# Optimization experiments

Measured on AMD Instinct MI355X. Metric: run time of the kernel, lower is better.

The kernel has to match this reference:

```python
import jax, jax.numpy as jnp
import numpy as np
import math

D_MODEL = 1024
D_STATE = 16
D_CONV = 4
EXPAND = 2
D_INNER = EXPAND * D_MODEL  # 2048
DT_RANK = 64
B_SZ = 2
L_SEQ = 1024


def setup_inputs() -> dict:
    key = jax.random.key(0)
    ks = jax.random.split(key, 10)
    x = jax.random.normal(ks[0], (B_SZ, L_SEQ, D_MODEL), dtype=jnp.float32)
    in_proj_w = jax.random.normal(ks[1], (2 * D_INNER, D_MODEL), dtype=jnp.float32) * (1.0 / math.sqrt(D_MODEL))
    conv_w = jax.random.normal(ks[2], (D_INNER, 1, D_CONV), dtype=jnp.float32) * (1.0 / math.sqrt(D_CONV))
    conv_b = jax.random.normal(ks[3], (D_INNER,), dtype=jnp.float32) * 0.01
    x_proj_w = jax.random.normal(ks[4], (DT_RANK + 2 * D_STATE, D_INNER), dtype=jnp.float32) * (1.0 / math.sqrt(D_INNER))
    dt_init_std = DT_RANK ** (-0.5)
    dt_proj_w = jax.random.uniform(ks[5], (D_INNER, DT_RANK), dtype=jnp.float32, minval=-dt_init_std, maxval=dt_init_std)
    dt = jnp.exp(jax.random.uniform(ks[6], (D_INNER,), dtype=jnp.float32) * (math.log(0.1) - math.log(0.001)) + math.log(0.001))
    dt = jnp.clip(dt, 1e-4, None)
    dt_proj_b = dt + jnp.log(-jnp.expm1(-dt))
    A_log = jnp.log(jnp.tile(jnp.arange(1, D_STATE + 1, dtype=jnp.float32)[None, :], (D_INNER, 1)))
    D = jnp.ones((D_INNER,), dtype=jnp.float32)
    out_proj_w = jax.random.normal(ks[7], (D_MODEL, D_INNER), dtype=jnp.float32) * (1.0 / math.sqrt(D_INNER))
    return {"x": x, "in_proj_w": in_proj_w, "conv_w": conv_w, "conv_b": conv_b,
            "x_proj_w": x_proj_w, "dt_proj_w": dt_proj_w, "dt_proj_b": dt_proj_b,
            "A_log": A_log, "D": D, "out_proj_w": out_proj_w}


def _mamba_forward(x, in_proj_w, conv_w, conv_b, x_proj_w, dt_proj_w, dt_proj_b, A_log, D, out_proj_w):
    B, L, _ = x.shape
    # input projection -> x, z each [B, L, Di]
    xz = jnp.einsum('bld,ed->ble', x, in_proj_w)
    xs, z = jnp.split(xz, 2, axis=-1)
    # causal depthwise conv along L (torch pads K-1 both sides then trims -> left pad only)
    xc = jnp.transpose(xs, (0, 2, 1))  # [B, Di, L]
    xc = jax.lax.conv_general_dilated(
        xc, conv_w, window_strides=(1,), padding=[(D_CONV - 1, 0)],
        feature_group_count=D_INNER, dimension_numbers=('NCH', 'OIH', 'NCH'))
    xc = xc + conv_b[None, :, None]
    xs = jnp.transpose(xc, (0, 2, 1))  # [B, L, Di]
    xs = jax.nn.silu(xs)
    # SSM parameters
    A = -jnp.exp(A_log)  # [Di, N]
    dbc = jnp.einsum('bld,ed->ble', xs, x_proj_w)
    delta_r = dbc[..., :DT_RANK]
    Bm = dbc[..., DT_RANK:DT_RANK + D_STATE]       # [B, L, N]
    Cm = dbc[..., DT_RANK + D_STATE:]              # [B, L, N]
    delta = jnp.einsum('blr,dr->bld', delta_r, dt_proj_w)
    delta = jax.nn.softplus(delta + dt_proj_b)     # [B, L, Di]
    # selective scan: h_t = exp(delta*A)*h_{t-1} + delta*B*x
    dA = jnp.exp(delta[..., None] * A)                          # [B, L, Di, N]
    dBx = (delta * xs)[..., None] * Bm[:, :, None, :]           # [B, L, Di, N]
    dA_t = jnp.moveaxis(dA, 1, 0)    # [L, B, Di, N]
    dBx_t = jnp.moveaxis(dBx, 1, 0)
    C_t = jnp.moveaxis(Cm, 1, 0)     # [L, B, N]
    h0 = jnp.zeros((B, D_INNER, D_STATE), dtype=xs.dtype)

    def step(h, inp):
        da, bx, c = inp
        h = da * h + bx
        y = jnp.einsum('bdn,bn->bd', h, c)
        return h, y

    _, ys = jax.lax.scan(step, h0, (dA_t, dBx_t, C_t))
    y = jnp.moveaxis(ys, 0, 1)       # [B, L, Di]
    y = y + D * xs
    # gating and output projection
    out = y * jax.nn.silu(z)
    return jnp.einsum('bld,od->blo', out, out_proj_w)


def reference(x, in_proj_w, conv_w, conv_b, x_proj_w, dt_proj_w, dt_proj_b, A_log, D, out_proj_w):
    return _mamba_forward(x, in_proj_w, conv_w, conv_b, x_proj_w, dt_proj_w, dt_proj_b, A_log, D, out_proj_w)
```

## Files before the change

### kernel.cpp

```cpp
#include <hip/hip_runtime.h>
#include <hip/hip_bf16.h>

typedef __attribute__((ext_vector_type(8))) short short8;
typedef __attribute__((ext_vector_type(4))) float f32x4;
typedef __hip_bfloat16 bf16;

#define D_MODEL 1024
#define D_INNER 2048
#define DT_RANK 64
#define D_STATE 16
#define B_SZ 2
#define L_SEQ 1024
#define NSEG 64
#define SL 16

__device__ __forceinline__ float b2f(bf16 x){ return __bfloat162float(x); }
__device__ __forceinline__ bf16  f2b(float x){ return __float2bfloat16(x); }

__device__ __forceinline__ void cvt_store8(bf16* dst, const float* s){
  union { short8 v; bf16 e[8]; } u;
  #pragma unroll
  for (int i = 0; i < 8; i++) u.e[i] = f2b(s[i]);
  *(short8*)dst = u.v;
}

__device__ __forceinline__ void gl_lds16(const bf16* g, bf16* l){
  __builtin_amdgcn_global_load_lds((const __attribute__((address_space(1))) unsigned int*)g,
                                   (__attribute__((address_space(3))) unsigned int*)l, 16, 0, 0);
}

__global__ __launch_bounds__(256) void cvt5_k(const float* s0, bf16* d0, int c0,
                                              const float* s1, bf16* d1, int c1,
                                              const float* s2, bf16* d2, int c2,
                                              const float* s3, bf16* d3, int c3,
                                              const float* s4, bf16* d4, int c4)
{
  int i = blockIdx.x * 256 + threadIdx.x;
  const float* s; bf16* d; int off;
  if      (i < c0) { s = s0; d = d0; off = i; }
  else if (i < c1) { s = s1; d = d1; off = i - c0; }
  else if (i < c2) { s = s2; d = d2; off = i - c1; }
  else if (i < c3) { s = s3; d = d3; off = i - c2; }
  else if (i < c4) { s = s4; d = d4; off = i - c3; }
  else return;
  float b[8];
  *(float4*)&b[0] = *(const float4*)(s + (size_t)off * 8);
  *(float4*)&b[4] = *(const float4*)(s + (size_t)off * 8 + 4);
  cvt_store8(d + (size_t)off * 8, b);
}

template<int MODE, int JT>
__global__ __launch_bounds__(256) void gemm_glds(const bf16* __restrict__ A,
                                                 const bf16* __restrict__ B,
                                                 void* __restrict__ Cout,
                                                 const float* __restrict__ bias,
                                                 int M, int N, int K)
{
  constexpr int BN = JT * 32;
  constexpr int BI = BN / 64;
  __shared__ bf16 As[128 * 32];
  __shared__ bf16 Bs[BN * 32];
  const int bm = blockIdx.y * 128, bn = blockIdx.x * BN;
  const int tid  = threadIdx.x;
  const int lane = tid & 63, wave = tid >> 6;
  const int wm = (wave & 1) * 64, wn = (wave >> 1) * (JT * 16);
  const int r = lane & 15, q = lane >> 4;

  const bf16* asrc[2];
  #pragma unroll
  for (int i = 0; i < 2; i++) {
    int c = i * 256 + tid;
    asrc[i] = A + (size_t)(bm + (c >> 2)) * K + (c & 3) * 8;
  }
  const bf16* bsrc[BI];
  #pragma unroll
  for (int i = 0; i < BI; i++) {
    int c = i * 256 + tid;
    bsrc[i] = B + (size_t)(bn + (c >> 2)) * K + (c & 3) * 8;
  }

  f32x4 acc[4][JT];
  #pragma unroll
  for (int i = 0; i < 4; i++)
    #pragma unroll
    for (int j = 0; j < JT; j++) acc[i][j] = (f32x4){0.f,0.f,0.f,0.f};

  for (int k0 = 0; k0 < K; k0 += 32) {
    #pragma unroll
    for (int i = 0; i < 2; i++)
      gl_lds16(asrc[i] + k0, &As[(i * 256 + tid) * 8]);
    #pragma unroll
    for (int i = 0; i < BI; i++)
      gl_lds16(bsrc[i] + k0, &Bs[(i * 256 + tid) * 8]);
    __syncthreads();
    short8 af[4], bfr[JT];
    #pragma unroll
    for (int i = 0; i < 4; i++)  af[i]  = *(const short8*)&As[(wm + i*16 + r) * 32 + q*8];
    #pragma unroll
    for (int j = 0; j < JT; j++) bfr[j] = *(const short8*)&Bs[(wn + j*16 + r) * 32 + q*8];
    #pragma unroll
    for (int j = 0; j < JT; j++)
      #pragma unroll
      for (int i = 0; i < 4; i++)
        acc[i][j] = __builtin_amdgcn_mfma_f32_16x16x32_bf16(af[i], bfr[j], acc[i][j], 0, 0, 0);
    __syncthreads();
  }

  #pragma unroll
  for (int i = 0; i < 4; i++)
    #pragma unroll
    for (int j = 0; j < JT; j++)
      #pragma unroll
      for (int t = 0; t < 4; t++) {
        int row = bm + wm + i*16 + q*4 + t;
        int col = bn + wn + j*16 + r;
        float v = acc[i][j][t];
        if (MODE == 0) {
          ((float*)Cout)[(size_t)row * N + col] = v;
        } else {
          ((bf16*)Cout)[(size_t)row * N + col] = f2b(v);
        }
      }
}

__global__ __launch_bounds__(256) void gemm_dt(const bf16* __restrict__ A,
                                               const bf16* __restrict__ W,
                                               float* __restrict__ Cout,
                                               const float* __restrict__ bias,
                                               int M, int N)
{
  const int lane = threadIdx.x & 63, wave = threadIdx.x >> 6;
  const int ntg  = N >> 6;
  const int task = blockIdx.x * 4 + wave;
  const int mt   = task / ntg;
  const int ng   = task - mt * ntg;
  const int r = lane & 15, q = lane >> 4;

  const bf16* pa = A + (size_t)(mt*16 + r) * DT_RANK + q*8;
  short8 a0 = *(const short8*)pa;
  short8 a1 = *(const short8*)(pa + 32);

  f32x4 acc[4];
  #pragma unroll
  for (int j = 0; j < 4; j++) {
    const bf16* pb = W + (size_t)(ng*64 + j*16 + r) * DT_RANK + q*8;
    short8 b0 = *(const short8*)pb;
    short8 b1 = *(const short8*)(pb + 32);
    f32x4 c = {0.f,0.f,0.f,0.f};
    c = __builtin_amdgcn_mfma_f32_16x16x32_bf16(a0, b0, c, 0, 0, 0);
    c = __builtin_amdgcn_mfma_f32_16x16x32_bf16(a1, b1, c, 0, 0, 0);
    acc[j] = c;
  }

  #pragma unroll
  for (int j = 0; j < 4; j++) {
    int col = ng*64 + j*16 + r;
    float bv = bias[col];
    #pragma unroll
    for (int t = 0; t < 4; t++) {
      int row = mt*16 + q*4 + t;
      float xv = acc[j][t] + bv;
      float sp = (xv > 20.f) ? xv : log1pf(__expf(xv));
      Cout[(size_t)row * N + col] = sp;
    }
  }
}

__global__ __launch_bounds__(256) void gemm_xproj(const bf16* __restrict__ A,
                                                  const bf16* __restrict__ W,
                                                  float* __restrict__ dbc,
                                                  bf16* __restrict__ dr)
{
  const int K = D_INNER;
  const int lane = threadIdx.x & 63, wave = threadIdx.x >> 6;
  const int mt = blockIdx.y * 4 + wave;
  const int nt = blockIdx.x;
  const int r = lane & 15, q = lane >> 4;
  const bf16* pa = A + (size_t)(mt*16 + r) * K + q*8;
  const bf16* pb = W + (size_t)(nt*16 + r) * K + q*8;
  f32x4 a0 = {0.f,0.f,0.f,0.f}, a1 = a0, a2 = a0, a3 = a0;
  for (int k0 = 0; k0 < K; k0 += 128) {
    short8 x0 = *(const short8*)(pa + k0);
    short8 w0 = *(const short8*)(pb + k0);
    short8 x1 = *(const short8*)(pa + k0 + 32);
    short8 w1 = *(const short8*)(pb + k0 + 32);
    short8 x2 = *(const short8*)(pa + k0 + 64);
    short8 w2 = *(const short8*)(pb + k0 + 64);
    short8 x3 = *(const short8*)(pa + k0 + 96);
    short8 w3 = *(const short8*)(pb + k0 + 96);
    a0 = __builtin_amdgcn_mfma_f32_16x16x32_bf16(x0, w0, a0, 0, 0, 0);
    a1 = __builtin_amdgcn_mfma_f32_16x16x32_bf16(x1, w1, a1, 0, 0, 0);
    a2 = __builtin_amdgcn_mfma_f32_16x16x32_bf16(x2, w2, a2, 0, 0, 0);
    a3 = __builtin_amdgcn_mfma_f32_16x16x32_bf16(x3, w3, a3, 0, 0, 0);
  }
  f32x4 acc = (a0 + a1) + (a2 + a3);
  #pragma unroll
  for (int t = 0; t < 4; t++) {
    int row = mt*16 + q*4 + t;
    int col = nt*16 + r;
    dbc[(size_t)row * 96 + col] = acc[t];
    if (col < DT_RANK) dr[(size_t)row * DT_RANK + col] = f2b(acc[t]);
  }
}

__global__ __launch_bounds__(256) void conv_silu_k(const bf16* __restrict__ xz,
                                                   const float* __restrict__ cw,
                                                   const float* __restrict__ cb,
                                                   bf16* __restrict__ xs_b)
{
  int idx = blockIdx.x * 256 + threadIdx.x;
  int d  = idx & (D_INNER - 1);
  int bl = idx >> 11;
  int l  = bl & (L_SEQ - 1);
  float acc = cb[d];
  #pragma unroll
  for (int j = 0; j < 4; ++j) {
    int lp = l - 3 + j;
    if (lp >= 0) acc += cw[d*4 + j] * b2f(xz[(size_t)(bl - 3 + j) * (2*D_INNER) + d]);
  }
  float s = acc / (1.f + __expf(-acc));
  xs_b[idx] = f2b(s);
}

__global__ __launch_bounds__(256) void scan_pass1(const float* __restrict__ delta,
                                                  const bf16* __restrict__ xs,
                                                  const float* __restrict__ dbc,
                                                  const float* __restrict__ A_log,
                                                  float* __restrict__ hseg,
                                                  float* __restrict__ Stot)
{
  __shared__ float bcs[SL][32];
  const int d   = blockIdx.x * 256 + threadIdx.x;
  const int seg = blockIdx.y, b = blockIdx.z;
  for (int i = threadIdx.x; i < SL*32; i += 256) {
    int l = i >> 5, c = i & 31;
    bcs[l][c] = dbc[((size_t)b*L_SEQ + seg*SL + l)*96 + DT_RANK + c];
  }
  __syncthreads();
  float An[16], h[16];
  #pragma unroll
  for (int n = 0; n < 16; n++) { An[n] = -__expf(A_log[d*16 + n]); h[n] = 0.f; }
  float S = 0.f;
  for (int li = 0; li < SL; ++li) {
    size_t bl = (size_t)b * L_SEQ + seg*SL + li;
    float dv = delta[bl*D_INNER + d];
    float xv = b2f(xs[bl*D_INNER + d]);
    S += dv;
    float dx = dv * xv;
    #pragma unroll
    for (int n = 0; n < 16; n++)
      h[n] = __expf(dv * An[n]) * h[n] + dx * bcs[li][n];
  }
  float* hp = hseg + (((size_t)seg*B_SZ + b)*D_INNER + d) * 16;
  #pragma unroll
  for (int n = 0; n < 16; n++) hp[n] = h[n];
  Stot[((size_t)seg*B_SZ + b)*D_INNER + d] = S;
}

__global__ __launch_bounds__(256) void scan_combine(const float* __restrict__ Stot,
                                                    float* __restrict__ hseg,
                                                    const float* __restrict__ A_log)
{
  int idx = blockIdx.x * 256 + threadIdx.x;
  int n = idx & 15;
  int d = (idx >> 4) & (D_INNER - 1);
  int b = idx >> 15;
  float An = -__expf(A_log[d*16 + n]);
  float H = 0.f;
  for (int s = 0; s < NSEG; s++) {
    size_t base = ((size_t)s*B_SZ + b)*D_INNER + d;
    float St   = Stot[base];
    float hloc = hseg[base*16 + n];
    hseg[base*16 + n] = H;
    H = __expf(An*St)*H + hloc;
  }
}

__global__ __launch_bounds__(256) void scan_pass3(const float* __restrict__ delta,
                                                  const bf16* __restrict__ xs,
                                                  const float* __restrict__ dbc,
                                                  const float* __restrict__ A_log,
                                                  const float* __restrict__ hseg,
                                                  const bf16* __restrict__ xz,
                                                  const float* __restrict__ Dw,
                                                  bf16* __restrict__ outin)
{
  __shared__ float bcs[SL][32];
  const int d   = blockIdx.x * 256 + threadIdx.x;
  const int seg = blockIdx.y, b = blockIdx.z;
  for (int i = threadIdx.x; i < SL*32; i += 256) {
    int l = i >> 5, c = i & 31;
    bcs[l][c] = dbc[((size_t)b*L_SEQ + seg*SL + l)*96 + DT_RANK + c];
  }
  __syncthreads();
  float An[16], h[16];
  const float* hp = hseg + (((size_t)seg*B_SZ + b)*D_INNER + d) * 16;
  #pragma unroll
  for (int n = 0; n < 16; n++) { An[n] = -__expf(A_log[d*16 + n]); h[n] = hp[n]; }
  const float Dv = Dw[d];
  for (int li = 0; li < SL; ++li) {
    size_t bl = (size_t)b * L_SEQ + seg*SL + li;
    float dv = delta[bl*D_INNER + d];
    float xv = b2f(xs[bl*D_INNER + d]);
    float dx = dv * xv;
    float y = 0.f;
    #pragma unroll
    for (int n = 0; n < 16; n++) {
      h[n] = __expf(dv * An[n]) * h[n] + dx * bcs[li][n];
      y   += h[n] * bcs[li][16 + n];
    }
    y += Dv * xv;
    float z = b2f(xz[bl*(size_t)(2*D_INNER) + D_INNER + d]);
    float g = z / (1.f + __expf(-z));
    outin[bl*D_INNER + d] = f2b(y * g);
  }
}

extern "C" void kernel_launch(void* const* d_in, const int* in_sizes, int n_in,
                              void* d_out, int out_size, void* d_ws, size_t ws_size,
                              hipStream_t stream)
{
  const float* x      = (const float*)d_in[0];
  const float* in_w   = (const float*)d_in[1];
  const float* conv_w = (const float*)d_in[2];
  const float* conv_b = (const float*)d_in[3];
  const float* xp_w   = (const float*)d_in[4];
  const float* dt_w   = (const float*)d_in[5];
  const float* dt_b   = (const float*)d_in[6];
  const float* A_log  = (const float*)d_in[7];
  const float* Dw     = (const float*)d_in[8];
  const float* out_w  = (const float*)d_in[9];
  float* out = (float*)d_out;

  char* p = (char*)d_ws;
  bf16*  xz    = (bf16*)p;  p += (size_t)B_SZ*L_SEQ*2*D_INNER*2;
  bf16*  xs_b  = (bf16*)p;  p += (size_t)B_SZ*L_SEQ*D_INNER*2;
  float* dbc   = (float*)p; p += (size_t)B_SZ*L_SEQ*96*4;
  bf16*  dr    = (bf16*)p;  p += (size_t)B_SZ*L_SEQ*DT_RANK*2;
  float* delta = (float*)p; p += (size_t)B_SZ*L_SEQ*D_INNER*4;
  float* Stot  = (float*)p; p += (size_t)NSEG*B_SZ*D_INNER*4;
  bf16*  outin = (bf16*)p;  p += (size_t)B_SZ*L_SEQ*D_INNER*2;
  bf16*  xp_wb = (bf16*)p;  p += (size_t)(DT_RANK+2*D_STATE)*D_INNER*2;
  bf16*  dt_wb = (bf16*)p;  p += (size_t)D_INNER*DT_RANK*2;
  bf16*  ow_b  = (bf16*)p;  p += (size_t)D_MODEL*D_INNER*2;
  char* u = p;
  bf16*  xb    = (bf16*)u;
  bf16*  in_wb = (bf16*)(u + (size_t)B_SZ*L_SEQ*D_MODEL*2);
  float* hseg  = (float*)u;
  p += (size_t)NSEG*B_SZ*D_INNER*16*4;

  const int M = B_SZ * L_SEQ;

  cvt5_k<<<4256, 256, 0, stream>>>(x, xb, 262144,
                                   in_w, in_wb, 786432,
                                   xp_w, xp_wb, 811008,
                                   dt_w, dt_wb, 827392,
                                   out_w, ow_b, 1089536);
  gemm_glds<2,4><<<dim3(2*D_INNER/128, M/128), 256, 0, stream>>>(xb, in_wb, xz, nullptr, M, 2*D_INNER, D_MODEL);
  conv_silu_k<<<(M*D_INNER)/256, 256, 0, stream>>>(xz, conv_w, conv_b, xs_b);
  gemm_xproj<<<dim3(6, M/64), 256, 0, stream>>>(xs_b, xp_wb, dbc, dr);
  gemm_dt<<<(M/16)*(D_INNER/64)/4, 256, 0, stream>>>(dr, dt_wb, delta, dt_b, M, D_INNER);
  scan_pass1<<<dim3(D_INNER/256, NSEG, B_SZ), 256, 0, stream>>>(delta, xs_b, dbc, A_log, hseg, Stot);
  scan_combine<<<(B_SZ*D_INNER*16)/256, 256, 0, stream>>>(Stot, hseg, A_log);
  scan_pass3<<<dim3(D_INNER/256, NSEG, B_SZ), 256, 0, stream>>>(delta, xs_b, dbc, A_log, hseg, xz, Dw, outin);
  gemm_glds<0,2><<<dim3(D_MODEL/64, M/128), 256, 0, stream>>>(outin, ow_b, out, nullptr, M, D_MODEL, D_INNER);
}
```

Measured before the change: 262.5 us.

## Stage GEMM epilogues through LDS, vectorize conv, and halve scan segment count

The two tiled GEMMs now write their accumulators into shared memory and copy them out as coalesced 16-byte row stores instead of scattered scalar stores. The dt GEMM does the same with a per-wave staging buffer. The depthwise conv+SiLU kernel now handles 8 channels per thread using vector loads and stores. The scan uses 32 segments of length 32 instead of 64 of 16, which means fewer combine states but longer serial segments. The cost is extra LDS traffic and syncs in the epilogues and less parallelism in the scan passes.

Result: slower. 268.8 us (+2.4%).

```diff
diff --git a/kernel.cpp b/kernel.cpp
--- a/kernel.cpp
+++ b/kernel.cpp
@@ -11,8 +11,8 @@
 #define D_STATE 16
 #define B_SZ 2
 #define L_SEQ 1024
-#define NSEG 64
-#define SL 16
+#define NSEG 32
+#define SL 32
 
 __device__ __forceinline__ float b2f(bf16 x){ return __bfloat162float(x); }
 __device__ __forceinline__ bf16  f2b(float x){ return __float2bfloat16(x); }
@@ -53,13 +53,19 @@
 __global__ __launch_bounds__(256) void gemm_glds(const bf16* __restrict__ A,
                                                  const bf16* __restrict__ B,
                                                  void* __restrict__ Cout,
-                                                 const float* __restrict__ bias,
                                                  int M, int N, int K)
 {
   constexpr int BN = JT * 32;
   constexpr int BI = BN / 64;
-  __shared__ bf16 As[128 * 32];
-  __shared__ bf16 Bs[BN * 32];
+  constexpr int ES = (MODE == 0) ? 4 : 2;
+  static_assert(BN * ES == 256, "copy-out assumes 256B tile rows");
+  constexpr int ROWB = BN * ES + 16;
+  constexpr int STAGE_AB = 128*32*2 + BN*32*2;
+  constexpr int SMEM = (128 * ROWB > STAGE_AB) ? 128 * ROWB : STAGE_AB;
+  __shared__ __align__(16) char smem[SMEM];
+  bf16* As = (bf16*)smem;
+  bf16* Bs = (bf16*)(smem + 128*32*2);
+
   const int bm = blockIdx.y * 128, bn = blockIdx.x * BN;
   const int tid  = threadIdx.x;
   const int lane = tid & 63, wave = tid >> 6;
@@ -112,15 +118,26 @@
     for (int j = 0; j < JT; j++)
       #pragma unroll
       for (int t = 0; t < 4; t++) {
-        int row = bm + wm + i*16 + q*4 + t;
-        int col = bn + wn + j*16 + r;
+        int lrow = wm + i*16 + q*4 + t;
+        int lcol = wn + j*16 + r;
         float v = acc[i][j][t];
-        if (MODE == 0) {
-          ((float*)Cout)[(size_t)row * N + col] = v;
-        } else {
-          ((bf16*)Cout)[(size_t)row * N + col] = f2b(v);
-        }
+        if (MODE == 0) *(float*)(smem + lrow*ROWB + lcol*4) = v;
+        else           *(bf16*)(smem + lrow*ROWB + lcol*2) = f2b(v);
       }
+  __syncthreads();
+  {
+    int row0 = tid >> 3, ch = tid & 7;
+    #pragma unroll
+    for (int rr = 0; rr < 4; rr++) {
+      int row = row0 + rr * 32;
+      const char* src = smem + row*ROWB + ch*32;
+      float4 w0 = *(const float4*)src;
+      float4 w1 = *(const float4*)(src + 16);
+      char* gdst = (char*)Cout + ((size_t)(bm + row) * N + bn) * ES + ch*32;
+      *(float4*)gdst        = w0;
+      *(float4*)(gdst + 16) = w1;
+    }
+  }
 }
 
 __global__ __launch_bounds__(256) void gemm_dt(const bf16* __restrict__ A,
@@ -129,6 +146,7 @@
                                                const float* __restrict__ bias,
                                                int M, int N)
 {
+  __shared__ __align__(16) float stg[4][16][68];
   const int lane = threadIdx.x & 63, wave = threadIdx.x >> 6;
   const int ntg  = N >> 6;
   const int task = blockIdx.x * 4 + wave;
@@ -140,7 +158,6 @@
   short8 a0 = *(const short8*)pa;
   short8 a1 = *(const short8*)(pa + 32);
 
-  f32x4 acc[4];
   #pragma unroll
   for (int j = 0; j < 4; j++) {
     const bf16* pb = W + (size_t)(ng*64 + j*16 + r) * DT_RANK + q*8;
@@ -149,20 +166,26 @@
     f32x4 c = {0.f,0.f,0.f,0.f};
     c = __builtin_amdgcn_mfma_f32_16x16x32_bf16(a0, b0, c, 0, 0, 0);
     c = __builtin_amdgcn_mfma_f32_16x16x32_bf16(a1, b1, c, 0, 0, 0);
-    acc[j] = c;
-  }
-
-  #pragma unroll
-  for (int j = 0; j < 4; j++) {
-    int col = ng*64 + j*16 + r;
-    float bv = bias[col];
+    float bv = bias[ng*64 + j*16 + r];
     #pragma unroll
     for (int t = 0; t < 4; t++) {
-      int row = mt*16 + q*4 + t;
-      float xv = acc[j][t] + bv;
+      float xv = c[t] + bv;
       float sp = (xv > 20.f) ? xv : log1pf(__expf(xv));
-      Cout[(size_t)row * N + col] = sp;
+      stg[wave][q*4 + t][j*16 + r] = sp;
     }
+  }
+  {
+    int row = lane >> 2, q4 = lane & 3;
+    const float* src = &stg[wave][row][q4 * 16];
+    float4 w0 = *(const float4*)(src);
+    float4 w1 = *(const float4*)(src + 4);
+    float4 w2 = *(const float4*)(src + 8);
+    float4 w3 = *(const float4*)(src + 12);
+    float* gdst = Cout + (size_t)(mt*16 + row) * N + ng*64 + q4*16;
+    *(float4*)(gdst)      = w0;
+    *(float4*)(gdst + 4)  = w1;
+    *(float4*)(gdst + 8)  = w2;
+    *(float4*)(gdst + 12) = w3;
   }
 }
 
@@ -209,17 +232,31 @@
                                                    bf16* __restrict__ xs_b)
 {
   int idx = blockIdx.x * 256 + threadIdx.x;
-  int d  = idx & (D_INNER - 1);
-  int bl = idx >> 11;
+  int dg = idx & (D_INNER/8 - 1);
+  int bl = idx >> 8;
   int l  = bl & (L_SEQ - 1);
-  float acc = cb[d];
+  int d0 = dg * 8;
+  const float4* cw4 = (const float4*)cw;
+  float4 w[8];
+  #pragma unroll
+  for (int i = 0; i < 8; i++) w[i] = cw4[d0 + i];
+  float acc[8];
+  #pragma unroll
+  for (int i = 0; i < 8; i++) acc[i] = cb[d0 + i];
   #pragma unroll
   for (int j = 0; j < 4; ++j) {
     int lp = l - 3 + j;
-    if (lp >= 0) acc += cw[d*4 + j] * b2f(xz[(size_t)(bl - 3 + j) * (2*D_INNER) + d]);
-  }
-  float s = acc / (1.f + __expf(-acc));
-  xs_b[idx] = f2b(s);
+    if (lp >= 0) {
+      short8 v = *(const short8*)(xz + (size_t)(bl - 3 + j) * (2*D_INNER) + d0);
+      #pragma unroll
+      for (int i = 0; i < 8; i++)
+        acc[i] += ((const float*)&w[i])[j] * b2f(((const bf16*)&v)[i]);
+    }
+  }
+  float o[8];
+  #pragma unroll
+  for (int i = 0; i < 8; i++) o[i] = acc[i] / (1.f + __expf(-acc[i]));
+  cvt_store8(xs_b + (size_t)idx * 8, o);
 }
 
 __global__ __launch_bounds__(256) void scan_pass1(const float* __restrict__ delta,
@@ -347,7 +384,7 @@
   bf16*  xb    = (bf16*)u;
   bf16*  in_wb = (bf16*)(u + (size_t)B_SZ*L_SEQ*D_MODEL*2);
   float* hseg  = (float*)u;
-  p += (size_t)NSEG*B_SZ*D_INNER*16*4;
+  p += (size_t)B_SZ*L_SEQ*(D_MODEL + 2*D_INNER)*2;
 
   const int M = B_SZ * L_SEQ;
 
@@ -356,12 +393,12 @@
                                    xp_w, xp_wb, 811008,
                                    dt_w, dt_wb, 827392,
                                    out_w, ow_b, 1089536);
-  gemm_glds<2,4><<<dim3(2*D_INNER/128, M/128), 256, 0, stream>>>(xb, in_wb, xz, nullptr, M, 2*D_INNER, D_MODEL);
-  conv_silu_k<<<(M*D_INNER)/256, 256, 0, stream>>>(xz, conv_w, conv_b, xs_b);
+  gemm_glds<2,4><<<dim3(2*D_INNER/128, M/128), 256, 0, stream>>>(xb, in_wb, xz, M, 2*D_INNER, D_MODEL);
+  conv_silu_k<<<(M*D_INNER/8)/256, 256, 0, stream>>>(xz, conv_w, conv_b, xs_b);
   gemm_xproj<<<dim3(6, M/64), 256, 0, stream>>>(xs_b, xp_wb, dbc, dr);
   gemm_dt<<<(M/16)*(D_INNER/64)/4, 256, 0, stream>>>(dr, dt_wb, delta, dt_b, M, D_INNER);
   scan_pass1<<<dim3(D_INNER/256, NSEG, B_SZ), 256, 0, stream>>>(delta, xs_b, dbc, A_log, hseg, Stot);
   scan_combine<<<(B_SZ*D_INNER*16)/256, 256, 0, stream>>>(Stot, hseg, A_log);
   scan_pass3<<<dim3(D_INNER/256, NSEG, B_SZ), 256, 0, stream>>>(delta, xs_b, dbc, A_log, hseg, xz, Dw, outin);
-  gemm_glds<0,2><<<dim3(D_MODEL/64, M/128), 256, 0, stream>>>(outin, ow_b, out, nullptr, M, D_MODEL, D_INNER);
-}
+  gemm_glds<0,2><<<dim3(D_MODEL/64, M/128), 256, 0, stream>>>(outin, ow_b, out, M, D_MODEL, D_INNER);
+}
```
